# Kernel tuning notes

Hardware: AMD Instinct MI355X
Metric: run time of the kernel (lower is better)

Reference implementation:

```python
import jax, jax.numpy as jnp
import numpy as np

N_NODES = 100000
N_EDGES = 1000000
D_IN, D_HID, D_OUT = 128, 128, 64
EPS = 1e-5


def setup_inputs() -> dict:
    key = jax.random.key(0)
    ks = jax.random.split(key, 10)
    x = jax.random.normal(ks[0], (N_NODES, D_IN), dtype=jnp.float32)
    edge_index = jax.random.randint(ks[1], (2, N_EDGES), 0, N_NODES, dtype=jnp.int64)
    # GCNConv weights (glorot-ish scale) and biases
    W0 = jax.random.normal(ks[2], (D_IN, D_HID), dtype=jnp.float32) / np.sqrt(D_IN)
    b0 = jnp.zeros((D_HID,), dtype=jnp.float32)
    W1 = jax.random.normal(ks[3], (D_HID, D_HID), dtype=jnp.float32) / np.sqrt(D_HID)
    b1 = jnp.zeros((D_HID,), dtype=jnp.float32)
    W2 = jax.random.normal(ks[4], (D_HID, D_OUT), dtype=jnp.float32) / np.sqrt(D_HID)
    b2 = jnp.zeros((D_OUT,), dtype=jnp.float32)
    # LayerNorm params for the n_layer-1 = 2 norm layers
    g0 = jnp.ones((D_HID,), dtype=jnp.float32)
    bn0 = jnp.zeros((D_HID,), dtype=jnp.float32)
    g1 = jnp.ones((D_HID,), dtype=jnp.float32)
    bn1 = jnp.zeros((D_HID,), dtype=jnp.float32)
    return {"x": x, "edge_index": edge_index, "W0": W0, "b0": b0,
            "W1": W1, "b1": b1, "W2": W2, "b2": b2,
            "g0": g0, "bn0": bn0, "g1": g1, "bn1": bn1}


def _gcn_norm(edge_index, n_nodes):
    # add self-loops, compute symmetric normalization deg^-1/2 * deg^-1/2
    loop = jnp.arange(n_nodes, dtype=edge_index.dtype)
    src = jnp.concatenate([edge_index[0], loop])
    dst = jnp.concatenate([edge_index[1], loop])
    deg = jax.ops.segment_sum(jnp.ones_like(dst, dtype=jnp.float32), dst,
                              num_segments=n_nodes)
    dinv = jnp.where(deg > 0, jax.lax.rsqrt(deg), 0.0)
    coef = dinv[src] * dinv[dst]  # [E + N]
    return src, dst, coef


def _gcn_conv(x, W, b, src, dst, coef, n_nodes):
    h = x @ W                              # [N, out]
    msg = h[src] * coef[:, None]           # gather + scale, [E+N, out]
    agg = jax.ops.segment_sum(msg, dst, num_segments=n_nodes)
    return agg + b


def _layer_norm(h, g, b):
    mu = jnp.mean(h, axis=-1, keepdims=True)
    var = jnp.mean(jnp.square(h - mu), axis=-1, keepdims=True)
    return (h - mu) * jax.lax.rsqrt(var + EPS) * g + b


def reference(x, edge_index, W0, b0, W1, b1, W2, b2, g0, bn0, g1, bn1):
    n = x.shape[0]
    src, dst, coef = _gcn_norm(edge_index, n)
    h = _gcn_conv(x, W0, b0, src, dst, coef, n)
    # layer 1 -> 2 (dropout is identity in eval mode)
    h = jax.nn.relu(_layer_norm(h, g0, bn0))
    h = _gcn_conv(h, W1, b1, src, dst, coef, n)
    # layer 2 -> 3
    h = jax.nn.relu(_layer_norm(h, g1, bn1))
    h = _gcn_conv(h, W2, b2, src, dst, coef, n)
    return h
```

## Files before the change

kernel.cpp:

```cpp
#include <hip/hip_runtime.h>
#include <hip/hip_bf16.h>
#include <stdint.h>

#define EPS 1e-5f
#define KPAD 136
#define NB 256

typedef __attribute__((ext_vector_type(8))) __bf16 bf16x8;
typedef __attribute__((ext_vector_type(4))) float f32x4;
typedef _Float16 f16;
typedef __attribute__((ext_vector_type(2))) _Float16 f16x2;
typedef __attribute__((ext_vector_type(8))) _Float16 f16x8;

__device__ __forceinline__ int rfl(int x) { return __builtin_amdgcn_readfirstlane(x); }
__device__ __forceinline__ float rflf(float x) {
    return __int_as_float(__builtin_amdgcn_readfirstlane(__float_as_int(x)));
}

__device__ __forceinline__ bool detect64(const uint32_t* w) {
    int lane = threadIdx.x & 63;
    uint32_t odd = w[1 + 2 * lane] | w[129 + 2 * lane];
    return !__any(odd != 0u);
}

__global__ __launch_bounds__(256) void k_scatter(const void* __restrict__ eidx,
                                                 int* __restrict__ cnt,
                                                 int* __restrict__ bcursor,
                                                 int2* __restrict__ bpairs,
                                                 int E, int shift, int cap) {
    __shared__ int hist[NB];
    __shared__ int base[NB];
    bool is64 = detect64((const uint32_t*)eidx);
    int t = threadIdx.x;
    if (t < NB) hist[t] = 0;
    __syncthreads();
    int e0 = blockIdx.x * 2048 + t * 8;
    int s[8], d[8], b[8], rank[8];
    #pragma unroll
    for (int i = 0; i < 8; i++) {
        int e = e0 + i;
        if (e < E) {
            if (is64) {
                const long long* p = (const long long*)eidx;
                s[i] = (int)p[e];
                d[i] = (int)p[(size_t)E + e];
            } else {
                const int* p = (const int*)eidx;
                s[i] = p[e];
                d[i] = p[(size_t)E + e];
            }
            b[i] = d[i] >> shift;
            rank[i] = atomicAdd(&hist[b[i]], 1);
            atomicAdd(&cnt[d[i]], 1);
        }
    }
    __syncthreads();
    if (t < NB) base[t] = hist[t] ? atomicAdd(&bcursor[t], hist[t]) : 0;
    __syncthreads();
    #pragma unroll
    for (int i = 0; i < 8; i++) {
        int e = e0 + i;
        if (e < E) {
            int idx = base[b[i]] + rank[i];
            if (idx < cap) bpairs[(size_t)b[i] * cap + idx] = make_int2(s[i], d[i]);
        }
    }
}

#define SCAN_CHUNK 2048
__global__ void k_scan1(const int* __restrict__ cnt, int* __restrict__ outp,
                        int* __restrict__ bsums, int N) {
    __shared__ int sm[256];
    int t = threadIdx.x;
    int base = blockIdx.x * SCAN_CHUNK + t * 8;
    int v[8];
    int s = 0;
    #pragma unroll
    for (int i = 0; i < 8; i++) {
        int idx = base + i;
        int x = (idx < N) ? cnt[idx] : 0;
        v[i] = s;
        s += x;
    }
    sm[t] = s;
    __syncthreads();
    for (int off = 1; off < 256; off <<= 1) {
        int tv = (t >= off) ? sm[t - off] : 0;
        __syncthreads();
        sm[t] += tv;
        __syncthreads();
    }
    int texcl = (t == 0) ? 0 : sm[t - 1];
    #pragma unroll
    for (int i = 0; i < 8; i++) {
        int idx = base + i;
        if (idx < N) outp[idx] = v[i] + texcl;
    }
    if (t == 255) bsums[blockIdx.x] = sm[255];
}

__global__ void k_scan2(int* __restrict__ bsums, int nb) {
    int lane = threadIdx.x;
    int carry = 0;
    for (int base = 0; base < nb; base += 64) {
        int i = base + lane;
        int v = (i < nb) ? bsums[i] : 0;
        int orig = v;
        #pragma unroll
        for (int off = 1; off < 64; off <<= 1) {
            int t = __shfl_up(v, off);
            if (lane >= off) v += t;
        }
        if (i < nb) bsums[i] = carry + v - orig;
        carry += __shfl(v, 63);
    }
}

__global__ void k_scan3_prep(int* __restrict__ rowptr, const int* __restrict__ bsums,
                             const int* __restrict__ cnt, int* __restrict__ cursor,
                             float* __restrict__ dinv, int N, int E) {
    int i = blockIdx.x * blockDim.x + threadIdx.x;
    if (i < N) {
        int rp = rowptr[i] + bsums[i / SCAN_CHUNK];
        rowptr[i] = rp;
        cursor[i] = rp;
        dinv[i] = rsqrtf((float)(cnt[i] + 1));
    }
    if (i == 0) rowptr[N] = E;
}

__global__ __launch_bounds__(256) void k_fill2(const int2* __restrict__ bpairs,
                                               const int* __restrict__ bcursor,
                                               int* __restrict__ cursor,
                                               int* __restrict__ adj, int cap) {
    int b = blockIdx.x;
    int n = bcursor[b];
    if (n > cap) n = cap;
    const int2* p = bpairs + (size_t)b * cap;
    for (int i = threadIdx.x; i < n; i += 256) {
        int2 pr = p[i];
        int pos = atomicAdd(&cursor[pr.y], 1);
        adj[pos] = pr.x;
    }
}

__global__ void k_wconv(const float* __restrict__ W0, const float* __restrict__ W1,
                        const float* __restrict__ W2, __bf16* __restrict__ T0,
                        __bf16* __restrict__ T1, __bf16* __restrict__ T2) {
    int layer = blockIdx.y;
    const float* W = layer == 0 ? W0 : (layer == 1 ? W1 : W2);
    __bf16* T = layer == 0 ? T0 : (layer == 1 ? T1 : T2);
    int outc = (layer == 2) ? 64 : 128;
    int tid = blockIdx.x * 256 + threadIdx.x;
    if (tid >= 128 * outc) return;
    int k = tid / outc, c = tid % outc;
    float f = W[tid];
    __bf16 hb = (__bf16)f;
    __bf16 lb = (__bf16)(f - (float)hb);
    T[c * KPAD + k] = hb;
    T[outc * KPAD + c * KPAD + k] = lb;
}

template <int OUTC, typename AT>
__global__ __launch_bounds__(256, 2) void k_gemm_mfma(const AT* __restrict__ A,
                                                      const __bf16* __restrict__ WT,
                                                      const float* __restrict__ dinv,
                                                      f16* __restrict__ C, int N) {
    __shared__ __bf16 lds[2 * OUTC * KPAD];
    const int t = threadIdx.x;
    const int n16 = (2 * OUTC * KPAD * 2) / 16;
    for (int i = t; i < n16; i += 256)
        ((float4*)lds)[i] = ((const float4*)WT)[i];

    const int lane = t & 63;
    const int wv = t >> 6;
    const int c = lane & 15;
    const int hq = lane >> 4;
    const int rowbase = blockIdx.x * 128 + wv * 32;

    bf16x8 ahi[2][4], alo[2][4];
    #pragma unroll
    for (int rt = 0; rt < 2; ++rt) {
        int ar = rowbase + rt * 16 + c;
        if (ar > N - 1) ar = N - 1;
        const AT* ap = A + (size_t)ar * 128 + hq * 8;
        #pragma unroll
        for (int ks = 0; ks < 4; ++ks) {
            float v[8];
            if constexpr (sizeof(AT) == 4) {
                float4 p = *(const float4*)(ap + ks * 32);
                float4 q = *(const float4*)(ap + ks * 32 + 4);
                v[0] = p.x; v[1] = p.y; v[2] = p.z; v[3] = p.w;
                v[4] = q.x; v[5] = q.y; v[6] = q.z; v[7] = q.w;
            } else {
                f16x8 r = *(const f16x8*)(ap + ks * 32);
                #pragma unroll
                for (int j = 0; j < 8; ++j) v[j] = (float)r[j];
            }
            #pragma unroll
            for (int j = 0; j < 8; ++j) {
                __bf16 hb = (__bf16)v[j];
                ahi[rt][ks][j] = hb;
                alo[rt][ks][j] = (__bf16)(v[j] - (float)hb);
            }
        }
    }
    float di[2][4];
    #pragma unroll
    for (int rt = 0; rt < 2; ++rt)
        #pragma unroll
        for (int r = 0; r < 4; ++r) {
            int row = rowbase + rt * 16 + hq * 4 + r;
            di[rt][r] = (row < N) ? dinv[row] : 0.f;
        }
    __syncthreads();

    #pragma unroll
    for (int ct = 0; ct < OUTC / 16; ++ct) {
        const __bf16* bp = &lds[(ct * 16 + c) * KPAD + hq * 8];
        bf16x8 bhi[4], blo[4];
        #pragma unroll
        for (int ks = 0; ks < 4; ++ks) {
            bhi[ks] = *reinterpret_cast<const bf16x8*>(bp + ks * 32);
            blo[ks] = *reinterpret_cast<const bf16x8*>(bp + OUTC * KPAD + ks * 32);
        }
        f32x4 acc0 = {0.f, 0.f, 0.f, 0.f};
        f32x4 acc1 = {0.f, 0.f, 0.f, 0.f};
        #pragma unroll
        for (int ks = 0; ks < 4; ++ks) {
            acc0 = __builtin_amdgcn_mfma_f32_16x16x32_bf16(ahi[0][ks], bhi[ks], acc0, 0, 0, 0);
            acc1 = __builtin_amdgcn_mfma_f32_16x16x32_bf16(ahi[1][ks], bhi[ks], acc1, 0, 0, 0);
            acc0 = __builtin_amdgcn_mfma_f32_16x16x32_bf16(alo[0][ks], bhi[ks], acc0, 0, 0, 0);
            acc1 = __builtin_amdgcn_mfma_f32_16x16x32_bf16(alo[1][ks], bhi[ks], acc1, 0, 0, 0);
            acc0 = __builtin_amdgcn_mfma_f32_16x16x32_bf16(ahi[0][ks], blo[ks], acc0, 0, 0, 0);
            acc1 = __builtin_amdgcn_mfma_f32_16x16x32_bf16(ahi[1][ks], blo[ks], acc1, 0, 0, 0);
        }
        const int col = ct * 16 + c;
        #pragma unroll
        for (int rt = 0; rt < 2; ++rt) {
            f32x4 a = rt ? acc1 : acc0;
            int row0 = rowbase + rt * 16 + hq * 4;
            #pragma unroll
            for (int r = 0; r < 4; ++r) {
                int row = row0 + r;
                if (row < N) C[(size_t)row * OUTC + col] = (f16)(a[r] * di[rt][r]);
            }
        }
    }
}

__global__ __launch_bounds__(256) void k_agg_ln(const f16* __restrict__ h,
                                                const int* __restrict__ rowptr,
                                                const int* __restrict__ adj,
                                                const float* __restrict__ dinv,
                                                const float* __restrict__ bias,
                                                const float* __restrict__ g,
                                                const float* __restrict__ bn,
                                                f16* __restrict__ out, int N) {
    int lane = threadIdx.x & 63;
    int v = rfl(blockIdx.x * 4 + (threadIdx.x >> 6));
    if (v >= N) return;
    int c = lane * 2;
    float dv = rflf(dinv[v]);
    f16x2 hv = *(const f16x2*)&h[(size_t)v * 128 + c];
    float ax = (float)hv[0];
    float ay = (float)hv[1];
    int e0 = rfl(rowptr[v]);
    int e1 = rfl(rowptr[v + 1]);
    int e = e0;
    for (; e + 16 <= e1; e += 16) {
        const f16* rp[16];
        #pragma unroll
        for (int i = 0; i < 16; i++) rp[i] = h + (size_t)rfl(adj[e + i]) * 128;
        f16x2 hh[16];
        #pragma unroll
        for (int i = 0; i < 16; i++) hh[i] = *(const f16x2*)&rp[i][c];
        #pragma unroll
        for (int i = 0; i < 16; i++) { ax += (float)hh[i][0]; ay += (float)hh[i][1]; }
    }
    for (; e + 4 <= e1; e += 4) {
        const f16* rp[4];
        #pragma unroll
        for (int i = 0; i < 4; i++) rp[i] = h + (size_t)rfl(adj[e + i]) * 128;
        f16x2 hh[4];
        #pragma unroll
        for (int i = 0; i < 4; i++) hh[i] = *(const f16x2*)&rp[i][c];
        #pragma unroll
        for (int i = 0; i < 4; i++) { ax += (float)hh[i][0]; ay += (float)hh[i][1]; }
    }
    for (; e < e1; e++) {
        const f16* rp = h + (size_t)rfl(adj[e]) * 128;
        f16x2 hu = *(const f16x2*)&rp[c];
        ax += (float)hu[0];
        ay += (float)hu[1];
    }
    float2 bb = *(const float2*)&bias[c];
    float px = fmaf(dv, ax, bb.x);
    float py = fmaf(dv, ay, bb.y);
    float s = px + py;
    #pragma unroll
    for (int m = 32; m >= 1; m >>= 1) s += __shfl_xor(s, m);
    float mu = s * (1.0f / 128.0f);
    float dx = px - mu, dy = py - mu;
    float vs = dx * dx + dy * dy;
    #pragma unroll
    for (int m = 32; m >= 1; m >>= 1) vs += __shfl_xor(vs, m);
    float rs = rsqrtf(vs * (1.0f / 128.0f) + EPS);
    float2 gg = *(const float2*)&g[c];
    float2 bnv = *(const float2*)&bn[c];
    float ox = fmaxf(dx * rs * gg.x + bnv.x, 0.0f);
    float oy = fmaxf(dy * rs * gg.y + bnv.y, 0.0f);
    f16x2 o;
    o[0] = (f16)ox;
    o[1] = (f16)oy;
    *(f16x2*)&out[(size_t)v * 128 + c] = o;
}

__global__ __launch_bounds__(256) void k_agg_out(const f16* __restrict__ h,
                                                 const int* __restrict__ rowptr,
                                                 const int* __restrict__ adj,
                                                 const float* __restrict__ dinv,
                                                 const float* __restrict__ bias,
                                                 float* __restrict__ out, int N) {
    int lane = threadIdx.x & 63;
    int v = rfl(blockIdx.x * 4 + (threadIdx.x >> 6));
    if (v >= N) return;
    float dv = rflf(dinv[v]);
    float acc = (float)h[(size_t)v * 64 + lane];
    int e0 = rfl(rowptr[v]);
    int e1 = rfl(rowptr[v + 1]);
    int e = e0;
    for (; e + 16 <= e1; e += 16) {
        const f16* rp[16];
        #pragma unroll
        for (int i = 0; i < 16; i++) rp[i] = h + (size_t)rfl(adj[e + i]) * 64;
        f16 hh[16];
        #pragma unroll
        for (int i = 0; i < 16; i++) hh[i] = rp[i][lane];
        #pragma unroll
        for (int i = 0; i < 16; i++) acc += (float)hh[i];
    }
    for (; e + 4 <= e1; e += 4) {
        const f16* rp[4];
        #pragma unroll
        for (int i = 0; i < 4; i++) rp[i] = h + (size_t)rfl(adj[e + i]) * 64;
        f16 hh[4];
        #pragma unroll
        for (int i = 0; i < 4; i++) hh[i] = rp[i][lane];
        #pragma unroll
        for (int i = 0; i < 4; i++) acc += (float)hh[i];
    }
    for (; e < e1; e++) {
        acc += (float)h[(size_t)rfl(adj[e]) * 64 + lane];
    }
    out[(size_t)v * 64 + lane] = fmaf(dv, acc, bias[lane]);
}

extern "C" void kernel_launch(void* const* d_in, const int* in_sizes, int n_in,
                              void* d_out, int out_size, void* d_ws, size_t ws_size,
                              hipStream_t stream) {
    const float* x    = (const float*)d_in[0];
    const void*  eidx = d_in[1];
    const float* W0 = (const float*)d_in[2];
    const float* b0 = (const float*)d_in[3];
    const float* W1 = (const float*)d_in[4];
    const float* b1 = (const float*)d_in[5];
    const float* W2 = (const float*)d_in[6];
    const float* b2 = (const float*)d_in[7];
    const float* g0 = (const float*)d_in[8];
    const float* bn0 = (const float*)d_in[9];
    const float* g1 = (const float*)d_in[10];
    const float* bn1 = (const float*)d_in[11];

    int N = in_sizes[0] / 128;
    int E = in_sizes[1] / 2;

    int shift = 0;
    while ((((N - 1) >> shift) + 1) > NB) shift++;
    int used = ((N - 1) >> shift) + 1;
    int cap = (E / used) * 2 + 256;

    char* p = (char*)d_ws;
    auto alloc = [&](size_t bytes) {
        char* r = p;
        p += (bytes + 255) & ~(size_t)255;
        return r;
    };
    int*   cnt     = (int*)alloc((size_t)N * 4);
    int*   rowptr  = (int*)alloc(((size_t)N + 1) * 4);
    int*   cursor  = (int*)alloc((size_t)N * 4);
    float* dinv    = (float*)alloc((size_t)N * 4);
    int*   adj     = (int*)alloc((size_t)E * 4);
    int2*  bpairs  = (int2*)alloc((size_t)used * cap * 8);
    int*   bcursor = (int*)alloc(NB * 4);
    int*   bsums   = (int*)alloc(4096);
    __bf16* wt0    = (__bf16*)alloc(2 * 128 * KPAD * 2);
    __bf16* wt1    = (__bf16*)alloc(2 * 128 * KPAD * 2);
    __bf16* wt2    = (__bf16*)alloc(2 * 64 * KPAD * 2);
    f16*   bufA    = (f16*)alloc((size_t)N * 128 * 2);
    f16*   bufB    = (f16*)alloc((size_t)N * 128 * 2);

    int nb = (N + 255) / 256;
    int nscan = (N + SCAN_CHUNK - 1) / SCAN_CHUNK;
    int sb = (E + 2047) / 2048;

    hipMemsetAsync(cnt, 0, (size_t)N * 4, stream);
    hipMemsetAsync(bcursor, 0, NB * 4, stream);
    k_wconv<<<dim3(64, 3), 256, 0, stream>>>(W0, W1, W2, wt0, wt1, wt2);
    k_scatter<<<sb, 256, 0, stream>>>(eidx, cnt, bcursor, bpairs, E, shift, cap);
    k_scan1<<<nscan, 256, 0, stream>>>(cnt, rowptr, bsums, N);
    k_scan2<<<1, 64, 0, stream>>>(bsums, nscan);
    k_scan3_prep<<<nb, 256, 0, stream>>>(rowptr, bsums, cnt, cursor, dinv, N, E);
    k_fill2<<<used, 256, 0, stream>>>(bpairs, bcursor, cursor, adj, cap);

    int gemmb = (N + 127) / 128;
    int aggb = (N + 3) / 4;

    k_gemm_mfma<128, float><<<gemmb, 256, 0, stream>>>(x, wt0, dinv, bufA, N);
    k_agg_ln<<<aggb, 256, 0, stream>>>(bufA, rowptr, adj, dinv, b0, g0, bn0, bufB, N);
    k_gemm_mfma<128, f16><<<gemmb, 256, 0, stream>>>(bufB, wt1, dinv, bufA, N);
    k_agg_ln<<<aggb, 256, 0, stream>>>(bufA, rowptr, adj, dinv, b1, g1, bn1, bufB, N);
    k_gemm_mfma<64, f16><<<gemmb, 256, 0, stream>>>(bufB, wt2, dinv, bufA, N);
    k_agg_out<<<aggb, 256, 0, stream>>>(bufA, rowptr, adj, dinv, b2, (float*)d_out, N);
}
```

Baseline: 310.7 us.

## Build CSR with per-bucket shared-memory histograms instead of global count scans

Fixes the destination bucket width at 512 nodes. The scatter kernel no longer does a global atomic increment per edge into a degree array. A new fill kernel computes per-node degrees, row pointers and dinv from a shared-memory histogram of each bucket, then places adjacency entries through shared-memory cursors, replacing three scan kernels and the global cursor atomics. The fixed bucket width assumes the node count is at most 256*512, so larger graphs would overflow the bucket arrays.

```diff
diff --git a/kernel.cpp b/kernel.cpp
--- a/kernel.cpp
+++ b/kernel.cpp
@@ -5,6 +5,7 @@
 #define EPS 1e-5f
 #define KPAD 136
 #define NB 256
+#define BSH 9
 
 typedef __attribute__((ext_vector_type(8))) __bf16 bf16x8;
 typedef __attribute__((ext_vector_type(4))) float f32x4;
@@ -24,10 +25,9 @@
 }
 
 __global__ __launch_bounds__(256) void k_scatter(const void* __restrict__ eidx,
-                                                 int* __restrict__ cnt,
-                                                 int* __restrict__ bcursor,
+                                                 int* __restrict__ bcount,
                                                  int2* __restrict__ bpairs,
-                                                 int E, int shift, int cap) {
+                                                 int E, int cap) {
     __shared__ int hist[NB];
     __shared__ int base[NB];
     bool is64 = detect64((const uint32_t*)eidx);
@@ -49,13 +49,12 @@
                 s[i] = p[e];
                 d[i] = p[(size_t)E + e];
             }
-            b[i] = d[i] >> shift;
+            b[i] = d[i] >> BSH;
             rank[i] = atomicAdd(&hist[b[i]], 1);
-            atomicAdd(&cnt[d[i]], 1);
-        }
-    }
-    __syncthreads();
-    if (t < NB) base[t] = hist[t] ? atomicAdd(&bcursor[t], hist[t]) : 0;
+        }
+    }
+    __syncthreads();
+    if (t < NB) base[t] = hist[t] ? atomicAdd(&bcount[t], hist[t]) : 0;
     __syncthreads();
     #pragma unroll
     for (int i = 0; i < 8; i++) {
@@ -67,80 +66,85 @@
     }
 }
 
-#define SCAN_CHUNK 2048
-__global__ void k_scan1(const int* __restrict__ cnt, int* __restrict__ outp,
-                        int* __restrict__ bsums, int N) {
-    __shared__ int sm[256];
-    int t = threadIdx.x;
-    int base = blockIdx.x * SCAN_CHUNK + t * 8;
-    int v[8];
-    int s = 0;
-    #pragma unroll
-    for (int i = 0; i < 8; i++) {
-        int idx = base + i;
-        int x = (idx < N) ? cnt[idx] : 0;
-        v[i] = s;
-        s += x;
-    }
-    sm[t] = s;
-    __syncthreads();
-    for (int off = 1; off < 256; off <<= 1) {
-        int tv = (t >= off) ? sm[t - off] : 0;
-        __syncthreads();
-        sm[t] += tv;
-        __syncthreads();
-    }
-    int texcl = (t == 0) ? 0 : sm[t - 1];
-    #pragma unroll
-    for (int i = 0; i < 8; i++) {
-        int idx = base + i;
-        if (idx < N) outp[idx] = v[i] + texcl;
-    }
-    if (t == 255) bsums[blockIdx.x] = sm[255];
-}
-
-__global__ void k_scan2(int* __restrict__ bsums, int nb) {
+__global__ void k_bscan(const int* __restrict__ bcount, int* __restrict__ bbase, int used) {
     int lane = threadIdx.x;
     int carry = 0;
-    for (int base = 0; base < nb; base += 64) {
+    for (int base = 0; base < used; base += 64) {
         int i = base + lane;
-        int v = (i < nb) ? bsums[i] : 0;
+        int v = (i < used) ? bcount[i] : 0;
         int orig = v;
         #pragma unroll
         for (int off = 1; off < 64; off <<= 1) {
             int t = __shfl_up(v, off);
             if (lane >= off) v += t;
         }
-        if (i < nb) bsums[i] = carry + v - orig;
+        if (i < used) bbase[i] = carry + v - orig;
         carry += __shfl(v, 63);
     }
 }
 
-__global__ void k_scan3_prep(int* __restrict__ rowptr, const int* __restrict__ bsums,
-                             const int* __restrict__ cnt, int* __restrict__ cursor,
-                             float* __restrict__ dinv, int N, int E) {
-    int i = blockIdx.x * blockDim.x + threadIdx.x;
-    if (i < N) {
-        int rp = rowptr[i] + bsums[i / SCAN_CHUNK];
-        rowptr[i] = rp;
-        cursor[i] = rp;
-        dinv[i] = rsqrtf((float)(cnt[i] + 1));
-    }
-    if (i == 0) rowptr[N] = E;
-}
-
-__global__ __launch_bounds__(256) void k_fill2(const int2* __restrict__ bpairs,
-                                               const int* __restrict__ bcursor,
-                                               int* __restrict__ cursor,
-                                               int* __restrict__ adj, int cap) {
+__global__ __launch_bounds__(256) void k_fill3(const int2* __restrict__ bpairs,
+                                               const int* __restrict__ bcount,
+                                               const int* __restrict__ bbase,
+                                               int* __restrict__ rowptr,
+                                               float* __restrict__ dinv,
+                                               int* __restrict__ adj,
+                                               int N, int E, int cap) {
+    __shared__ int hist[512];
+    __shared__ int wsum[4];
+    __shared__ int wexcl[4];
     int b = blockIdx.x;
-    int n = bcursor[b];
+    int t = threadIdx.x;
+    int lane = t & 63;
+    int wv = t >> 6;
+    int d0 = b << BSH;
+    int W = N - d0;
+    if (W > 512) W = 512;
+    int n = bcount[b];
     if (n > cap) n = cap;
+    int base = bbase[b];
     const int2* p = bpairs + (size_t)b * cap;
-    for (int i = threadIdx.x; i < n; i += 256) {
+
+    hist[t] = 0;
+    hist[t + 256] = 0;
+    __syncthreads();
+    for (int i = t; i < n; i += 256) atomicAdd(&hist[p[i].y - d0], 1);
+    __syncthreads();
+    int i0 = 2 * t, i1 = 2 * t + 1;
+    int a = hist[i0], bv = hist[i1];
+    int s2 = a + bv;
+    int incl = s2;
+    #pragma unroll
+    for (int off = 1; off < 64; off <<= 1) {
+        int tv = __shfl_up(incl, off);
+        if (lane >= off) incl += tv;
+    }
+    if (lane == 63) wsum[wv] = incl;
+    __syncthreads();
+    if (t == 0) {
+        int r = 0;
+        #pragma unroll
+        for (int i = 0; i < 4; i++) { wexcl[i] = r; r += wsum[i]; }
+    }
+    __syncthreads();
+    int excl = incl - s2 + wexcl[wv];
+    if (i0 < W) {
+        rowptr[d0 + i0] = base + excl;
+        dinv[d0 + i0] = rsqrtf((float)(a + 1));
+    }
+    if (i1 < W) {
+        rowptr[d0 + i1] = base + excl + a;
+        dinv[d0 + i1] = rsqrtf((float)(bv + 1));
+    }
+    if (b == gridDim.x - 1 && t == 0) rowptr[N] = E;
+    __syncthreads();
+    hist[i0] = excl;
+    hist[i1] = excl + a;
+    __syncthreads();
+    for (int i = t; i < n; i += 256) {
         int2 pr = p[i];
-        int pos = atomicAdd(&cursor[pr.y], 1);
-        adj[pos] = pr.x;
+        int pos = atomicAdd(&hist[pr.y - d0], 1);
+        adj[base + pos] = pr.x;
     }
 }
 
@@ -375,9 +379,7 @@
     int N = in_sizes[0] / 128;
     int E = in_sizes[1] / 2;
 
-    int shift = 0;
-    while ((((N - 1) >> shift) + 1) > NB) shift++;
-    int used = ((N - 1) >> shift) + 1;
+    int used = ((N - 1) >> BSH) + 1;
     int cap = (E / used) * 2 + 256;
 
     char* p = (char*)d_ws;
@@ -386,32 +388,25 @@
         p += (bytes + 255) & ~(size_t)255;
         return r;
     };
-    int*   cnt     = (int*)alloc((size_t)N * 4);
     int*   rowptr  = (int*)alloc(((size_t)N + 1) * 4);
-    int*   cursor  = (int*)alloc((size_t)N * 4);
     float* dinv    = (float*)alloc((size_t)N * 4);
     int*   adj     = (int*)alloc((size_t)E * 4);
     int2*  bpairs  = (int2*)alloc((size_t)used * cap * 8);
-    int*   bcursor = (int*)alloc(NB * 4);
-    int*   bsums   = (int*)alloc(4096);
+    int*   bcount  = (int*)alloc(NB * 4);
+    int*   bbase   = (int*)alloc(NB * 4);
     __bf16* wt0    = (__bf16*)alloc(2 * 128 * KPAD * 2);
     __bf16* wt1    = (__bf16*)alloc(2 * 128 * KPAD * 2);
     __bf16* wt2    = (__bf16*)alloc(2 * 64 * KPAD * 2);
     f16*   bufA    = (f16*)alloc((size_t)N * 128 * 2);
     f16*   bufB    = (f16*)alloc((size_t)N * 128 * 2);
 
-    int nb = (N + 255) / 256;
-    int nscan = (N + SCAN_CHUNK - 1) / SCAN_CHUNK;
     int sb = (E + 2047) / 2048;
 
-    hipMemsetAsync(cnt, 0, (size_t)N * 4, stream);
-    hipMemsetAsync(bcursor, 0, NB * 4, stream);
+    hipMemsetAsync(bcount, 0, NB * 4, stream);
     k_wconv<<<dim3(64, 3), 256, 0, stream>>>(W0, W1, W2, wt0, wt1, wt2);
-    k_scatter<<<sb, 256, 0, stream>>>(eidx, cnt, bcursor, bpairs, E, shift, cap);
-    k_scan1<<<nscan, 256, 0, stream>>>(cnt, rowptr, bsums, N);
-    k_scan2<<<1, 64, 0, stream>>>(bsums, nscan);
-    k_scan3_prep<<<nb, 256, 0, stream>>>(rowptr, bsums, cnt, cursor, dinv, N, E);
-    k_fill2<<<used, 256, 0, stream>>>(bpairs, bcursor, cursor, adj, cap);
+    k_scatter<<<sb, 256, 0, stream>>>(eidx, bcount, bpairs, E, cap);
+    k_bscan<<<1, 64, 0, stream>>>(bcount, bbase, used);
+    k_fill3<<<used, 256, 0, stream>>>(bpairs, bcount, bbase, rowptr, dinv, adj, N, E, cap);
 
     int gemmb = (N + 127) / 128;
     int aggb = (N + 3) / 4;
```

Result: faster. 257.9 us (-17.0%).
